# Kernel tuning notes

Measured on AMD Instinct MI355X. Metric: run time of the kernel, lower is better.

Reference implementation:

```python
import jax, jax.numpy as jnp
import numpy as np

B, T, D_IN, D_OUT = 8, 2048, 4096, 4096
N_ADAPTERS, R_MAX = 8, 64


def setup_inputs() -> dict:
    key = jax.random.key(0)
    k_x, k_base, k_idx, k_A, k_B, k_s = jax.random.split(key, 6)
    x = jax.random.normal(k_x, (B, T, D_IN), dtype=jnp.float32)
    base_output = jax.random.normal(k_base, (B, T, D_OUT), dtype=jnp.float32)
    adapter_indices = jax.random.randint(k_idx, (B,), 0, N_ADAPTERS, dtype=jnp.int64)
    # He-uniform init for A (kaiming_uniform with a=sqrt(5) -> bound = 1/sqrt(fan_in))
    bound = 1.0 / np.sqrt(D_IN)
    lora_A = jax.random.uniform(k_A, (N_ADAPTERS, D_IN, R_MAX), dtype=jnp.float32,
                                minval=-bound, maxval=bound)
    # lora_B is zeros at init; use small random values for a non-trivial reference
    lora_B = jax.random.normal(k_B, (N_ADAPTERS, R_MAX, D_OUT), dtype=jnp.float32) * 0.02
    lora_scaling = jax.random.uniform(k_s, (N_ADAPTERS,), dtype=jnp.float32,
                                      minval=0.5, maxval=2.0)
    return {"x": x, "base_output": base_output, "adapter_indices": adapter_indices,
            "lora_A": lora_A, "lora_B": lora_B, "lora_scaling": lora_scaling}


def reference(x, base_output, adapter_indices, lora_A, lora_B, lora_scaling):
    # Gather per-batch adapter weights (adapter index broadcasts over sequence):
    # equivalent to sort-by-adapter -> grouped GEMM -> unsort, since every token
    # in a batch row shares one adapter and all ranks equal r_max.
    A_b = lora_A[adapter_indices]          # [B, D_IN, R]
    B_b = lora_B[adapter_indices]          # [B, R, D_OUT]
    s_b = lora_scaling[adapter_indices]    # [B]
    inter = jnp.einsum('btd,bdr->btr', x, A_b)        # [B, T, R]
    y = jnp.einsum('btr,bro->bto', inter, B_b)        # [B, T, D_OUT]
    return base_output + y * s_b[:, None, None]
```

## Files before the change

### kernel.cpp

```cpp
#include <hip/hip_runtime.h>
#include <hip/hip_bf16.h>
#include <cstdint>
#include <cstddef>

#define BT    16384
#define DIN   4096
#define DOUT  4096
#define RR    64
#define TSEQ  2048
#define NADP  8

typedef float  f32x4  __attribute__((ext_vector_type(4)));
typedef __bf16 bf16x8 __attribute__((ext_vector_type(8)));

static __device__ __forceinline__ unsigned short bf16_bits(float f) {
    return __builtin_bit_cast(unsigned short, (__bf16)f);
}

static __device__ __forceinline__ size_t i2_idx(int mblk, int rb, int mrow, int j) {
    return ((((size_t)mblk * 8 + rb) * 16 + mrow) * 8 + j);
}

__global__ __launch_bounds__(256) void k_prep_a(
    const float* __restrict__ A, __bf16* __restrict__ At2)
{
    const int gtid = blockIdx.x * 256 + threadIdx.x;
    const int r  = gtid & 63;
    const int kb = (gtid >> 6) & (DIN / 8 - 1);
    const int a  = gtid >> 15;
    const float* __restrict__ src = A + (size_t)a * DIN * RR + (size_t)kb * 8 * RR + r;
    unsigned int u[4];
    #pragma unroll
    for (int p = 0; p < 4; ++p) {
        unsigned int lo = bf16_bits(src[(2 * p + 0) * RR]);
        unsigned int hi = bf16_bits(src[(2 * p + 1) * RR]);
        u[p] = lo | (hi << 16);
    }
    *(uint4*)&At2[(size_t)gtid * 8] = make_uint4(u[0], u[1], u[2], u[3]);
}

__global__ __launch_bounds__(256) void k_prep_b(
    const float* __restrict__ Bw, __bf16* __restrict__ Bp)
{
    const int gtid = blockIdx.x * 256 + threadIdx.x;
    const int o  = gtid & (DOUT - 1);
    const int rb = (gtid >> 12) & 7;
    const int a  = gtid >> 15;
    const float* __restrict__ src = Bw + (size_t)a * RR * DOUT + (size_t)rb * 8 * DOUT + o;
    unsigned int u[4];
    #pragma unroll
    for (int p = 0; p < 4; ++p) {
        unsigned int lo = bf16_bits(src[(2 * p + 0) * DOUT]);
        unsigned int hi = bf16_bits(src[(2 * p + 1) * DOUT]);
        u[p] = lo | (hi << 16);
    }
    *(uint4*)&Bp[(size_t)gtid * 8] = make_uint4(u[0], u[1], u[2], u[3]);
}

__global__ __launch_bounds__(256, 1) void k_xa(
    const float* __restrict__ x, const int* __restrict__ idx,
    const __bf16* __restrict__ At2, __bf16* __restrict__ inter2)
{
    const int m0   = blockIdx.x * 64;
    const int a    = idx[m0 / TSEQ];
    const int w    = threadIdx.x >> 6, lane = threadIdx.x & 63;
    const int mr   = lane & 15, kg = lane >> 4;
    const int mw   = m0 + w * 16;
    const float*  __restrict__ xrow = x   + (size_t)(mw + mr) * DIN + kg * 8;
    const __bf16* __restrict__ Aw   = At2 + (size_t)a * RR * DIN;

    f32x4 z = {0.f, 0.f, 0.f, 0.f};
    f32x4 acc[4] = {z, z, z, z};

    float4 px0[4], px1[4];
    bf16x8 pb[4][4];

    #pragma unroll
    for (int s = 0; s < 3; ++s) {
        px0[s] = *(const float4*)(xrow + s * 32);
        px1[s] = *(const float4*)(xrow + s * 32 + 4);
        #pragma unroll
        for (int n = 0; n < 4; ++n)
            pb[s][n] = *(const bf16x8*)&Aw[((size_t)(s * 4 + kg) * 64 + n * 16 + mr) * 8];
    }

    #pragma unroll 4
    for (int ks = 0; ks < 128; ++ks) {
        const int pf = ks + 3;
        const int sp = pf & 3, sc = ks & 3;
        if (pf < 128) {
            px0[sp] = *(const float4*)(xrow + pf * 32);
            px1[sp] = *(const float4*)(xrow + pf * 32 + 4);
            #pragma unroll
            for (int n = 0; n < 4; ++n)
                pb[sp][n] = *(const bf16x8*)&Aw[((size_t)(pf * 4 + kg) * 64 + n * 16 + mr) * 8];
        }
        float4 u0 = px0[sc], u1 = px1[sc];
        bf16x8 af;
        af[0] = (__bf16)u0.x; af[1] = (__bf16)u0.y;
        af[2] = (__bf16)u0.z; af[3] = (__bf16)u0.w;
        af[4] = (__bf16)u1.x; af[5] = (__bf16)u1.y;
        af[6] = (__bf16)u1.z; af[7] = (__bf16)u1.w;
        #pragma unroll
        for (int n = 0; n < 4; ++n)
            acc[n] = __builtin_amdgcn_mfma_f32_16x16x32_bf16(af, pb[sc][n], acc[n], 0, 0, 0);
    }

    const int mblk = blockIdx.x * 4 + w;
    #pragma unroll
    for (int n = 0; n < 4; ++n) {
        const int rb = n * 2 + (mr >> 3), j = mr & 7;
        #pragma unroll
        for (int q = 0; q < 4; ++q)
            inter2[i2_idx(mblk, rb, kg * 4 + q, j)] = (__bf16)acc[n][q];
    }
}

__global__ __launch_bounds__(256) void k_by(
    const __bf16* __restrict__ inter2, const float* __restrict__ base,
    const int* __restrict__ idx, const __bf16* __restrict__ Bp,
    const float* __restrict__ scal, float* __restrict__ out)
{
    const int o0 = blockIdx.x * 64;
    const int m0 = blockIdx.y * 64;
    const int a  = idx[m0 / TSEQ];
    const float s = scal[a];
    const __bf16* __restrict__ Ba = Bp + (size_t)a * RR * DOUT;
    const int lane = threadIdx.x & 63;
    const int w    = threadIdx.x >> 6;
    const int mr   = lane & 15, kg = lane >> 4;
    const int oc   = o0 + w * 16 + mr;

    f32x4 z = {0.f, 0.f, 0.f, 0.f};
    f32x4 acc[4] = {z, z, z, z};

    #pragma unroll
    for (int ksub = 0; ksub < 2; ++ksub) {
        const int rb = ksub * 4 + kg;
        bf16x8 bfA = *(const bf16x8*)&Ba[((size_t)rb * DOUT + oc) * 8];
        #pragma unroll
        for (int mt = 0; mt < 4; ++mt) {
            bf16x8 afB = *(const bf16x8*)&inter2[i2_idx(m0 / 16 + mt, rb, mr, 0)];
            acc[mt] = __builtin_amdgcn_mfma_f32_16x16x32_bf16(bfA, afB, acc[mt], 0, 0, 0);
        }
    }

    #pragma unroll
    for (int mt = 0; mt < 4; ++mt) {
        size_t off = (size_t)(m0 + mt * 16 + mr) * DOUT + o0 + w * 16 + kg * 4;
        float4 bv = *(const float4*)&base[off];
        float4 o;
        o.x = bv.x + s * acc[mt][0];
        o.y = bv.y + s * acc[mt][1];
        o.z = bv.z + s * acc[mt][2];
        o.w = bv.w + s * acc[mt][3];
        *(float4*)&out[off] = o;
    }
}

__global__ __launch_bounds__(256) void k_xa_fb(
    const float* __restrict__ x, const int* __restrict__ idx,
    const float* __restrict__ A, __bf16* __restrict__ inter)
{
    const int m0   = blockIdx.x * 32;
    const int a    = idx[m0 / TSEQ];
    const float* __restrict__ Aa = A + (size_t)a * DIN * RR;
    const int lane = threadIdx.x & 63;
    const int rw   = threadIdx.x >> 6;
    const int mr   = lane & 15, kg = lane >> 4;
    const int rcol = rw * 16 + mr;
    const float* __restrict__ xrow0 = x + (size_t)(m0 + mr) * DIN;
    const float* __restrict__ xrow1 = x + (size_t)(m0 + 16 + mr) * DIN;

    f32x4 acc0 = {0.f, 0.f, 0.f, 0.f};
    f32x4 acc1 = {0.f, 0.f, 0.f, 0.f};

    for (int k0 = 0; k0 < DIN; k0 += 64) {
        #pragma unroll
        for (int ksub = 0; ksub < 2; ++ksub) {
            const int koff = k0 + ksub * 32 + kg * 8;
            float4 u0 = *(const float4*)&xrow0[koff];
            float4 u1 = *(const float4*)&xrow0[koff + 4];
            float4 v0 = *(const float4*)&xrow1[koff];
            float4 v1 = *(const float4*)&xrow1[koff + 4];
            bf16x8 af0, af1;
            af0[0] = (__bf16)u0.x; af0[1] = (__bf16)u0.y;
            af0[2] = (__bf16)u0.z; af0[3] = (__bf16)u0.w;
            af0[4] = (__bf16)u1.x; af0[5] = (__bf16)u1.y;
            af0[6] = (__bf16)u1.z; af0[7] = (__bf16)u1.w;
            af1[0] = (__bf16)v0.x; af1[1] = (__bf16)v0.y;
            af1[2] = (__bf16)v0.z; af1[3] = (__bf16)v0.w;
            af1[4] = (__bf16)v1.x; af1[5] = (__bf16)v1.y;
            af1[6] = (__bf16)v1.z; af1[7] = (__bf16)v1.w;
            const float* ap = &Aa[(size_t)koff * RR + rcol];
            bf16x8 bf;
            bf[0] = (__bf16)ap[0 * RR]; bf[1] = (__bf16)ap[1 * RR];
            bf[2] = (__bf16)ap[2 * RR]; bf[3] = (__bf16)ap[3 * RR];
            bf[4] = (__bf16)ap[4 * RR]; bf[5] = (__bf16)ap[5 * RR];
            bf[6] = (__bf16)ap[6 * RR]; bf[7] = (__bf16)ap[7 * RR];
            acc0 = __builtin_amdgcn_mfma_f32_16x16x32_bf16(af0, bf, acc0, 0, 0, 0);
            acc1 = __builtin_amdgcn_mfma_f32_16x16x32_bf16(af1, bf, acc1, 0, 0, 0);
        }
    }
    #pragma unroll
    for (int q = 0; q < 4; ++q) {
        inter[(size_t)(m0 + kg * 4 + q) * RR + rcol]      = (__bf16)acc0[q];
        inter[(size_t)(m0 + 16 + kg * 4 + q) * RR + rcol] = (__bf16)acc1[q];
    }
}

__global__ __launch_bounds__(256) void k_by_fb(
    const __bf16* __restrict__ inter, const float* __restrict__ base,
    const int* __restrict__ idx, const float* __restrict__ Bw,
    const float* __restrict__ scal, float* __restrict__ out)
{
    const int o0 = blockIdx.x * 64;
    const int m0 = blockIdx.y * 64;
    const int a  = idx[m0 / TSEQ];
    const float s = scal[a];
    const float* __restrict__ Ba = Bw + (size_t)a * RR * DOUT;
    const int lane = threadIdx.x & 63;
    const int w    = threadIdx.x >> 6;
    const int mr   = lane & 15, kg = lane >> 4;
    const int oc   = o0 + w * 16 + mr;

    f32x4 z = {0.f, 0.f, 0.f, 0.f};
    f32x4 acc[4] = {z, z, z, z};

    #pragma unroll
    for (int ksub = 0; ksub < 2; ++ksub) {
        const int kb = ksub * 32 + kg * 8;
        const float* bp = &Ba[(size_t)kb * DOUT + oc];
        bf16x8 bf;
        bf[0] = (__bf16)bp[0 * DOUT]; bf[1] = (__bf16)bp[1 * DOUT];
        bf[2] = (__bf16)bp[2 * DOUT]; bf[3] = (__bf16)bp[3 * DOUT];
        bf[4] = (__bf16)bp[4 * DOUT]; bf[5] = (__bf16)bp[5 * DOUT];
        bf[6] = (__bf16)bp[6 * DOUT]; bf[7] = (__bf16)bp[7 * DOUT];
        #pragma unroll
        for (int mt = 0; mt < 4; ++mt) {
            bf16x8 af = *(const bf16x8*)&inter[(size_t)(m0 + mt * 16 + mr) * RR + kb];
            acc[mt] = __builtin_amdgcn_mfma_f32_16x16x32_bf16(af, bf, acc[mt], 0, 0, 0);
        }
    }
    #pragma unroll
    for (int mt = 0; mt < 4; ++mt) {
        #pragma unroll
        for (int q = 0; q < 4; ++q) {
            size_t off = (size_t)(m0 + mt * 16 + kg * 4 + q) * DOUT + oc;
            out[off] = base[off] + s * acc[mt][q];
        }
    }
}

extern "C" void kernel_launch(void* const* d_in, const int* in_sizes, int n_in,
                              void* d_out, int out_size, void* d_ws, size_t ws_size,
                              hipStream_t stream)
{
    const float* x    = (const float*)d_in[0];
    const float* base = (const float*)d_in[1];
    const int*   idx  = (const int*)  d_in[2];
    const float* A    = (const float*)d_in[3];
    const float* Bw   = (const float*)d_in[4];
    const float* scal = (const float*)d_in[5];
    float* out = (float*)d_out;

    const size_t INTER_B = (size_t)BT * RR * 2;
    const size_t AT_B    = (size_t)NADP * RR * DIN * 2;
    const size_t BT_B    = (size_t)NADP * DOUT * RR * 2;

    if (ws_size >= INTER_B + AT_B + BT_B) {
        __bf16* inter2 = (__bf16*)d_ws;
        __bf16* At2    = (__bf16*)((char*)d_ws + INTER_B);
        __bf16* Bp     = (__bf16*)((char*)d_ws + INTER_B + AT_B);
        k_prep_a<<<dim3(1024), 256, 0, stream>>>(A, At2);
        k_prep_b<<<dim3(1024), 256, 0, stream>>>(Bw, Bp);
        k_xa<<<dim3(BT / 64),            256, 0, stream>>>(x, idx, At2, inter2);
        k_by<<<dim3(DOUT / 64, BT / 64), 256, 0, stream>>>(inter2, base, idx, Bp, scal, out);
    } else {
        __bf16* inter = (__bf16*)d_ws;
        k_xa_fb<<<dim3(BT / 32),            256, 0, stream>>>(x, idx, A, inter);
        k_by_fb<<<dim3(DOUT / 64, BT / 64), 256, 0, stream>>>(inter, base, idx, Bw, scal, out);
    }
}
```

Before: 234.8 us.

## Stage x tiles through swizzled LDS with double buffering in k_xa

The x·A kernel now loads 64-wide fp32 chunks of x per row, converts them to bf16 and writes them into a per-wave, XOR-swizzled, double-buffered LDS tile. MFMA A-operands are read back from LDS while the next chunk's global loads are in flight. Previously each lane issued 32-float strided loads directly into a 4-deep register ring. This makes each global load request wider and more contiguous and lowers register pressure, at the cost of extra LDS traffic. Because each wave reads only the slice it wrote itself, no barriers are needed. The A-weight loads are no longer prefetched ahead and are issued inline in each step. The fallback kernel only gains a cvt8 helper refactor.

```diff
diff --git a/kernel.cpp b/kernel.cpp
--- a/kernel.cpp
+++ b/kernel.cpp
@@ -21,6 +21,13 @@
     return ((((size_t)mblk * 8 + rb) * 16 + mrow) * 8 + j);
 }
 
+static __device__ __forceinline__ bf16x8 cvt8(float4 a, float4 b) {
+    bf16x8 v;
+    v[0] = (__bf16)a.x; v[1] = (__bf16)a.y; v[2] = (__bf16)a.z; v[3] = (__bf16)a.w;
+    v[4] = (__bf16)b.x; v[5] = (__bf16)b.y; v[6] = (__bf16)b.z; v[7] = (__bf16)b.w;
+    return v;
+}
+
 __global__ __launch_bounds__(256) void k_prep_a(
     const float* __restrict__ A, __bf16* __restrict__ At2)
 {
@@ -61,50 +68,83 @@
     const float* __restrict__ x, const int* __restrict__ idx,
     const __bf16* __restrict__ At2, __bf16* __restrict__ inter2)
 {
+    __shared__ __bf16 xs[4][2][16][64];
+
     const int m0   = blockIdx.x * 64;
     const int a    = idx[m0 / TSEQ];
     const int w    = threadIdx.x >> 6, lane = threadIdx.x & 63;
     const int mr   = lane & 15, kg = lane >> 4;
-    const int mw   = m0 + w * 16;
-    const float*  __restrict__ xrow = x   + (size_t)(mw + mr) * DIN + kg * 8;
-    const __bf16* __restrict__ Aw   = At2 + (size_t)a * RR * DIN;
+
+    const float* __restrict__ xsrc = x + (size_t)(m0 + w * 16 + mr) * DIN;
+    const int sw1 = (kg     ^ (mr & 7)) * 8;
+    const int sw2 = ((kg+4) ^ (mr & 7)) * 8;
+    __bf16* const dE1 = &xs[w][0][mr][sw1];
+    __bf16* const dE2 = &xs[w][0][mr][sw2];
+    __bf16* const dO1 = &xs[w][1][mr][sw1];
+    __bf16* const dO2 = &xs[w][1][mr][sw2];
+
+    const __bf16* __restrict__ Aw = At2 + (size_t)a * RR * DIN;
 
     f32x4 z = {0.f, 0.f, 0.f, 0.f};
     f32x4 acc[4] = {z, z, z, z};
 
-    float4 px0[4], px1[4];
-    bf16x8 pb[4][4];
-
-    #pragma unroll
-    for (int s = 0; s < 3; ++s) {
-        px0[s] = *(const float4*)(xrow + s * 32);
-        px1[s] = *(const float4*)(xrow + s * 32 + 4);
-        #pragma unroll
-        for (int n = 0; n < 4; ++n)
-            pb[s][n] = *(const bf16x8*)&Aw[((size_t)(s * 4 + kg) * 64 + n * 16 + mr) * 8];
-    }
-
-    #pragma unroll 4
-    for (int ks = 0; ks < 128; ++ks) {
-        const int pf = ks + 3;
-        const int sp = pf & 3, sc = ks & 3;
-        if (pf < 128) {
-            px0[sp] = *(const float4*)(xrow + pf * 32);
-            px1[sp] = *(const float4*)(xrow + pf * 32 + 4);
-            #pragma unroll
-            for (int n = 0; n < 4; ++n)
-                pb[sp][n] = *(const bf16x8*)&Aw[((size_t)(pf * 4 + kg) * 64 + n * 16 + mr) * 8];
-        }
-        float4 u0 = px0[sc], u1 = px1[sc];
-        bf16x8 af;
-        af[0] = (__bf16)u0.x; af[1] = (__bf16)u0.y;
-        af[2] = (__bf16)u0.z; af[3] = (__bf16)u0.w;
-        af[4] = (__bf16)u1.x; af[5] = (__bf16)u1.y;
-        af[6] = (__bf16)u1.z; af[7] = (__bf16)u1.w;
-        #pragma unroll
-        for (int n = 0; n < 4; ++n)
-            acc[n] = __builtin_amdgcn_mfma_f32_16x16x32_bf16(af, pb[sc][n], acc[n], 0, 0, 0);
-    }
+    float4 e0, e1, e2, e3, o0, o1, o2, o3;
+
+    e0 = *(const float4*)(xsrc + 0 * 64 + kg * 8);
+    e1 = *(const float4*)(xsrc + 0 * 64 + kg * 8 + 4);
+    e2 = *(const float4*)(xsrc + 0 * 64 + (kg + 4) * 8);
+    e3 = *(const float4*)(xsrc + 0 * 64 + (kg + 4) * 8 + 4);
+    o0 = *(const float4*)(xsrc + 1 * 64 + kg * 8);
+    o1 = *(const float4*)(xsrc + 1 * 64 + kg * 8 + 4);
+    o2 = *(const float4*)(xsrc + 1 * 64 + (kg + 4) * 8);
+    o3 = *(const float4*)(xsrc + 1 * 64 + (kg + 4) * 8 + 4);
+    *(bf16x8*)dE1 = cvt8(e0, e1);
+    *(bf16x8*)dE2 = cvt8(e2, e3);
+
+#define COMPUTE(BUF, T)                                                        \
+    {                                                                          \
+        bf16x8 b00 = *(const bf16x8*)&Aw[(((size_t)(T)*8 + 0*4 + kg)*64 +  0 + mr)*8]; \
+        bf16x8 b01 = *(const bf16x8*)&Aw[(((size_t)(T)*8 + 0*4 + kg)*64 + 16 + mr)*8]; \
+        bf16x8 b02 = *(const bf16x8*)&Aw[(((size_t)(T)*8 + 0*4 + kg)*64 + 32 + mr)*8]; \
+        bf16x8 b03 = *(const bf16x8*)&Aw[(((size_t)(T)*8 + 0*4 + kg)*64 + 48 + mr)*8]; \
+        bf16x8 b10 = *(const bf16x8*)&Aw[(((size_t)(T)*8 + 1*4 + kg)*64 +  0 + mr)*8]; \
+        bf16x8 b11 = *(const bf16x8*)&Aw[(((size_t)(T)*8 + 1*4 + kg)*64 + 16 + mr)*8]; \
+        bf16x8 b12 = *(const bf16x8*)&Aw[(((size_t)(T)*8 + 1*4 + kg)*64 + 32 + mr)*8]; \
+        bf16x8 b13 = *(const bf16x8*)&Aw[(((size_t)(T)*8 + 1*4 + kg)*64 + 48 + mr)*8]; \
+        bf16x8 af0 = *(const bf16x8*)&xs[w][BUF][mr][((0*4 + kg) ^ (mr & 7)) * 8];     \
+        bf16x8 af1 = *(const bf16x8*)&xs[w][BUF][mr][((1*4 + kg) ^ (mr & 7)) * 8];     \
+        acc[0] = __builtin_amdgcn_mfma_f32_16x16x32_bf16(af0, b00, acc[0], 0, 0, 0);   \
+        acc[1] = __builtin_amdgcn_mfma_f32_16x16x32_bf16(af0, b01, acc[1], 0, 0, 0);   \
+        acc[2] = __builtin_amdgcn_mfma_f32_16x16x32_bf16(af0, b02, acc[2], 0, 0, 0);   \
+        acc[3] = __builtin_amdgcn_mfma_f32_16x16x32_bf16(af0, b03, acc[3], 0, 0, 0);   \
+        acc[0] = __builtin_amdgcn_mfma_f32_16x16x32_bf16(af1, b10, acc[0], 0, 0, 0);   \
+        acc[1] = __builtin_amdgcn_mfma_f32_16x16x32_bf16(af1, b11, acc[1], 0, 0, 0);   \
+        acc[2] = __builtin_amdgcn_mfma_f32_16x16x32_bf16(af1, b12, acc[2], 0, 0, 0);   \
+        acc[3] = __builtin_amdgcn_mfma_f32_16x16x32_bf16(af1, b13, acc[3], 0, 0, 0);   \
+    }
+
+    for (int t2 = 0; t2 < 32; ++t2) {
+        const int t   = 2 * t2;
+        const int tp2 = (t + 2 <= 63) ? (t + 2) : 63;
+        const int tp3 = (t + 3 <= 63) ? (t + 3) : 63;
+
+        e0 = *(const float4*)(xsrc + tp2 * 64 + kg * 8);
+        e1 = *(const float4*)(xsrc + tp2 * 64 + kg * 8 + 4);
+        e2 = *(const float4*)(xsrc + tp2 * 64 + (kg + 4) * 8);
+        e3 = *(const float4*)(xsrc + tp2 * 64 + (kg + 4) * 8 + 4);
+        COMPUTE(0, t)
+        *(bf16x8*)dO1 = cvt8(o0, o1);
+        *(bf16x8*)dO2 = cvt8(o2, o3);
+
+        o0 = *(const float4*)(xsrc + tp3 * 64 + kg * 8);
+        o1 = *(const float4*)(xsrc + tp3 * 64 + kg * 8 + 4);
+        o2 = *(const float4*)(xsrc + tp3 * 64 + (kg + 4) * 8);
+        o3 = *(const float4*)(xsrc + tp3 * 64 + (kg + 4) * 8 + 4);
+        COMPUTE(1, t + 1)
+        *(bf16x8*)dE1 = cvt8(e0, e1);
+        *(bf16x8*)dE2 = cvt8(e2, e3);
+    }
+#undef COMPUTE
 
     const int mblk = blockIdx.x * 4 + w;
     #pragma unroll
@@ -183,15 +223,8 @@
             float4 u1 = *(const float4*)&xrow0[koff + 4];
             float4 v0 = *(const float4*)&xrow1[koff];
             float4 v1 = *(const float4*)&xrow1[koff + 4];
-            bf16x8 af0, af1;
-            af0[0] = (__bf16)u0.x; af0[1] = (__bf16)u0.y;
-            af0[2] = (__bf16)u0.z; af0[3] = (__bf16)u0.w;
-            af0[4] = (__bf16)u1.x; af0[5] = (__bf16)u1.y;
-            af0[6] = (__bf16)u1.z; af0[7] = (__bf16)u1.w;
-            af1[0] = (__bf16)v0.x; af1[1] = (__bf16)v0.y;
-            af1[2] = (__bf16)v0.z; af1[3] = (__bf16)v0.w;
-            af1[4] = (__bf16)v1.x; af1[5] = (__bf16)v1.y;
-            af1[6] = (__bf16)v1.z; af1[7] = (__bf16)v1.w;
+            bf16x8 af0 = cvt8(u0, u1);
+            bf16x8 af1 = cvt8(v0, v1);
             const float* ap = &Aa[(size_t)koff * RR + rcol];
             bf16x8 bf;
             bf[0] = (__bf16)ap[0 * RR]; bf[1] = (__bf16)ap[1 * RR];
```

Measured after the change: 216.9 us. 1.08x faster.
